# Kernel optimization log

Hardware: AMD Instinct MI355X
Metric: run time of the kernel (lower is better)

## Reference

```python
import jax, jax.numpy as jnp
import numpy as np

N_EMB = 1024
N_HEAD = 16
HD = N_EMB // N_HEAD
ROPE_BASE = 10000.0


def _rope_cos_sin(seq_len, dim, dtype):
    inv_freq = 1.0 / (ROPE_BASE ** (jnp.arange(0, dim, 2, dtype=jnp.float32) / dim))
    t = jnp.arange(seq_len, dtype=jnp.float32)
    freqs = jnp.outer(t, inv_freq)              # [S, dim/2]
    emb = jnp.concatenate([freqs, freqs], -1)    # [S, dim]
    return jnp.cos(emb).astype(dtype), jnp.sin(emb).astype(dtype)


def _rotate_half(x):
    x1, x2 = jnp.split(x, 2, axis=-1)
    return jnp.concatenate([-x2, x1], axis=-1)


def _apply_rope(x):
    # x: [B, H, L, hd]; rotary over sequence axis (-2)
    cos, sin = _rope_cos_sin(x.shape[-2], x.shape[-1], x.dtype)
    return x * cos + _rotate_half(x) * sin


def setup_inputs() -> dict:
    key = jax.random.key(0)
    ks = jax.random.split(key, 8)
    B, T, S = 2, 2048, 2048
    std = 0.02
    return {
        "x": jax.random.normal(ks[0], (B, T, N_EMB), jnp.float32),
        "memory": jax.random.normal(ks[1], (B, S, N_EMB), jnp.float32),
        "q_w": jax.random.normal(ks[2], (N_EMB, N_EMB), jnp.float32) * std,
        "q_b": jnp.zeros((N_EMB,), jnp.float32),
        "kv_w": jax.random.normal(ks[3], (N_EMB, 2 * N_EMB), jnp.float32) * std,
        "kv_b": jnp.zeros((2 * N_EMB,), jnp.float32),
        "proj_w": jax.random.normal(ks[4], (N_EMB, N_EMB), jnp.float32) * std,
        "proj_b": jnp.zeros((N_EMB,), jnp.float32),
    }


def reference(x, memory, q_w, q_b, kv_w, kv_b, proj_w, proj_b):
    B, S, C = memory.shape
    T = x.shape[1]
    kv = memory @ kv_w + kv_b                      # [B,S,2C]
    K, V = jnp.split(kv, 2, axis=-1)
    Q = x @ q_w + q_b                              # [B,T,C]

    def heads(t, L):
        return t.reshape(B, L, N_HEAD, HD).transpose(0, 2, 1, 3)

    Q, K, V = heads(Q, T), heads(K, S), heads(V, S)
    Q = jax.nn.elu(Q) + 1.0                        # positive feature map
    K = jax.nn.elu(K) + 1.0
    Q_rot = _apply_rope(Q)
    K_rot = _apply_rope(K)
    # denom row-sum: sum_s Q.K_s == Q . (sum_s K_s) -- identical math, no SxT matrix
    denom = jnp.einsum('bhtd,bhd->bht', Q, K.sum(axis=2))[..., None]  # [B,H,T,1]
    att = jnp.einsum('bhtd,bhsd->bhts', Q_rot, K_rot) / denom          # [B,H,T,S]
    y = jnp.einsum('bhts,bhsd->bhtd', att, V)                          # [B,H,T,hd]
    y = y.transpose(0, 2, 1, 3).reshape(B, T, C)
    return y @ proj_w + proj_b
```

## Files before the change

kernel.cpp:

```cpp
#include <hip/hip_runtime.h>
#include <cstddef>
#include <cstdint>

#define B_SZ  2
#define T_SEQ 2048
#define S_SEQ 2048
#define C_EMB 1024
#define NH    16
#define HD    64
#define KDIM  1024

typedef __attribute__((ext_vector_type(8))) short bf16x8;
typedef __attribute__((ext_vector_type(4))) float f32x4;

#define OFF_XH    ((size_t)0)
#define OFF_XL    ((size_t)2097152)
#define OFF_MEMH  ((size_t)4194304)
#define OFF_MEML  ((size_t)6291456)
#define OFF_QWH   ((size_t)8388608)
#define OFF_QWL   ((size_t)8912896)
#define OFF_KVWH  ((size_t)9437184)
#define OFF_KVWL  ((size_t)10485760)
#define OFF_PWH   ((size_t)11534336)
#define OFF_PWL   ((size_t)12058624)
#define OFF_KSUM  ((size_t)12582912)
#define OFF_MT    ((size_t)12584960)
#define OFF_TAB   ((size_t)12716032)
#define OFF_YH    ((size_t)12847104)
#define OFF_YL    ((size_t)14944256)
#define WS_FLOATS ((size_t)17041408)

__device__ __forceinline__ float elu1(float v) {
    return v > 0.0f ? v + 1.0f : __expf(v);
}
__device__ __forceinline__ unsigned short bf16_rne(float x) {
    union { float f; unsigned int u; } v; v.f = x;
    unsigned int u = v.u;
    return (unsigned short)((u + 0x7FFFu + ((u >> 16) & 1u)) >> 16);
}
__device__ __forceinline__ float bf16_to_f(unsigned short h) {
    union { unsigned int u; float f; } v; v.u = ((unsigned int)h) << 16;
    return v.f;
}

#define PREP_BLOCKS 13064

__device__ __forceinline__ void split4_body(
    const float4* __restrict__ in, ushort4* __restrict__ hi,
    ushort4* __restrict__ lo, int i)
{
    float4 v = in[i];
    ushort4 h, l;
    h.x = bf16_rne(v.x); l.x = bf16_rne(v.x - bf16_to_f(h.x));
    h.y = bf16_rne(v.y); l.y = bf16_rne(v.y - bf16_to_f(h.y));
    h.z = bf16_rne(v.z); l.z = bf16_rne(v.z - bf16_to_f(h.z));
    h.w = bf16_rne(v.w); l.w = bf16_rne(v.w - bf16_to_f(h.w));
    hi[i] = h; lo[i] = l;
}

__device__ __forceinline__ void transpose_body(
    const float* __restrict__ W, unsigned short* __restrict__ Wth,
    unsigned short* __restrict__ Wtl, int K, int N, int bx, int by,
    float (*tile)[33])
{
    const int k0 = by * 32, n0 = bx * 32;
    const int tx = threadIdx.x & 31, ty = threadIdx.x >> 5;
    #pragma unroll
    for (int j = 0; j < 4; ++j)
        tile[ty + j * 8][tx] = W[(size_t)(k0 + ty + j * 8) * N + n0 + tx];
    __syncthreads();
    #pragma unroll
    for (int j = 0; j < 4; ++j) {
        float x = tile[tx][ty + j * 8];
        unsigned short h = bf16_rne(x);
        unsigned short l = bf16_rne(x - bf16_to_f(h));
        size_t o = (size_t)(n0 + ty + j * 8) * K + k0 + tx;
        Wth[o] = h; Wtl[o] = l;
    }
}

__global__ __launch_bounds__(256) void prep_kernel(
    const float* __restrict__ x, const float* __restrict__ memory,
    const float* __restrict__ q_w, const float* __restrict__ kv_w,
    const float* __restrict__ proj_w,
    unsigned short* __restrict__ xh, unsigned short* __restrict__ xl,
    unsigned short* __restrict__ mh, unsigned short* __restrict__ ml,
    unsigned short* __restrict__ qwh, unsigned short* __restrict__ qwl,
    unsigned short* __restrict__ kvwh, unsigned short* __restrict__ kvwl,
    unsigned short* __restrict__ pwh, unsigned short* __restrict__ pwl,
    float2* __restrict__ tab, float* __restrict__ zero_base)
{
    __shared__ float tile[32][33];
    const int bid = blockIdx.x;
    const int tid = threadIdx.x;
    if (bid < 4096) {
        split4_body((const float4*)x, (ushort4*)xh, (ushort4*)xl, bid * 256 + tid);
    } else if (bid < 8192) {
        split4_body((const float4*)memory, (ushort4*)mh, (ushort4*)ml, (bid - 4096) * 256 + tid);
    } else if (bid < 9216) {
        int i = bid - 8192;
        transpose_body(q_w, qwh, qwl, 1024, 1024, i & 31, i >> 5, tile);
    } else if (bid < 11264) {
        int i = bid - 9216;
        transpose_body(kv_w, kvwh, kvwl, 1024, 2048, i & 63, i >> 6, tile);
    } else if (bid < 12288) {
        int i = bid - 11264;
        transpose_body(proj_w, pwh, pwl, 1024, 1024, i & 31, i >> 5, tile);
    } else if (bid < 12544) {
        int idx = (bid - 12288) * 256 + tid;
        int pos = idx >> 5, i = idx & 31;
        double invf = exp(-(double)i * (9.210340371976184 / 32.0));
        float arg = (float)((double)pos * invf);
        float sn, cs;
        sincosf(arg, &sn, &cs);
        tab[idx] = make_float2(cs, sn);
    } else {
        int idx = (bid - 12544) * 256 + tid;
        if (idx < 2048 + 131072) zero_base[idx] = 0.0f;
    }
}

#define WAITCNT_VM(N) asm volatile("s_waitcnt vmcnt(" #N ")" ::: "memory")
#define WAIT_LGKM0()  asm volatile("s_waitcnt lgkmcnt(0)" ::: "memory")

template<int BN, int M_IT, bool KV>
__device__ __forceinline__ void gemm_pipe(
    const unsigned short* __restrict__ Ah, const unsigned short* __restrict__ Al,
    const unsigned short* __restrict__ Bth, const unsigned short* __restrict__ Btl,
    unsigned short* lds, int m0, int n0, f32x4 (&acc)[M_IT][4])
{
    constexpr int BUFSZ = 16384 + 2 * BN * 32;
    constexpr int NT = KDIM / 32;
    const int tid = threadIdx.x;
    const int w = tid >> 6, lane = tid & 63;
    const int quad = lane >> 4, lrow = lane & 15;
    const int sr = tid >> 2;
    const int g  = (tid & 3) ^ ((tid >> 3) & 3);
    constexpr int WAVES_N = (BN == 128) ? 2 : 1;
    const int wr = (WAVES_N == 2) ? (w >> 1) : w;
    const int wc = (WAVES_N == 2) ? (w & 1) : 0;
    const int rowbase = wr * (M_IT * 16);
    const int colbase = wc * 64;
    const int sw = ((quad ^ ((lrow >> 1) & 3)) << 3);

    const unsigned short* gA0 = Ah + (size_t)(m0 + sr) * KDIM + g * 8;
    const unsigned short* gA1 = Ah + (size_t)(m0 + 128 + sr) * KDIM + g * 8;
    const unsigned short* gA2 = Al + (size_t)(m0 + sr) * KDIM + g * 8;
    const unsigned short* gA3 = Al + (size_t)(m0 + 128 + sr) * KDIM + g * 8;
    const unsigned short* gB0;
    const unsigned short* gB1 = nullptr;
    if constexpr (KV) {
        size_t brow = (size_t)(n0 + sr) + (sr >= 64 ? (size_t)960 : 0);
        gB0 = Bth + brow * KDIM + g * 8;
        gB1 = Btl + brow * KDIM + g * 8;
    } else {
        const unsigned short* bsrc = (w < 4) ? Bth : Btl;
        gB0 = bsrc + (size_t)(n0 + (sr & 63)) * KDIM + g * 8;
    }
    const int lA0 = w * 512;
    const int lA1 = 4096 + w * 512;
    const int lA2 = 8192 + w * 512;
    const int lA3 = 12288 + w * 512;
    int lB0, lB1 = 0;
    if constexpr (KV) {
        lB0 = 16384 + w * 512;
        lB1 = 20480 + w * 512;
    } else {
        lB0 = 16384 + ((w >= 4) ? 2048 : 0) + (w & 3) * 512;
    }

    auto STAGE = [&](unsigned short* buf, int k0) {
        __builtin_amdgcn_global_load_lds(
            (const __attribute__((address_space(1))) unsigned int*)(gA0 + k0),
            (__attribute__((address_space(3))) unsigned int*)(buf + lA0), 16, 0, 0);
        __builtin_amdgcn_global_load_lds(
            (const __attribute__((address_space(1))) unsigned int*)(gA1 + k0),
            (__attribute__((address_space(3))) unsigned int*)(buf + lA1), 16, 0, 0);
        __builtin_amdgcn_global_load_lds(
            (const __attribute__((address_space(1))) unsigned int*)(gA2 + k0),
            (__attribute__((address_space(3))) unsigned int*)(buf + lA2), 16, 0, 0);
        __builtin_amdgcn_global_load_lds(
            (const __attribute__((address_space(1))) unsigned int*)(gA3 + k0),
            (__attribute__((address_space(3))) unsigned int*)(buf + lA3), 16, 0, 0);
        __builtin_amdgcn_global_load_lds(
            (const __attribute__((address_space(1))) unsigned int*)(gB0 + k0),
            (__attribute__((address_space(3))) unsigned int*)(buf + lB0), 16, 0, 0);
        if constexpr (KV)
            __builtin_amdgcn_global_load_lds(
                (const __attribute__((address_space(1))) unsigned int*)(gB1 + k0),
                (__attribute__((address_space(3))) unsigned int*)(buf + lB1), 16, 0, 0);
    };

    unsigned short* cur = lds;
    unsigned short* nxt = lds + BUFSZ;
    unsigned short* thr = lds + 2 * BUFSZ;
    STAGE(cur, 0);
    STAGE(nxt, 32);

    #pragma unroll 1
    for (int t = 0; t < NT; ++t) {
        if (t == NT - 1) {
            WAITCNT_VM(0);
        } else {
            if constexpr (KV) { WAITCNT_VM(6); } else { WAITCNT_VM(5); }
        }
        __builtin_amdgcn_s_barrier();

        bf16x8 ah[M_IT], al[M_IT];
        #pragma unroll
        for (int it = 0; it < M_IT; ++it) {
            int off = (rowbase + it * 16 + lrow) * 32 + sw;
            ah[it] = *(const bf16x8*)&cur[off];
            al[it] = *(const bf16x8*)&cur[8192 + off];
        }
        bf16x8 bh[2], bl[2];
        #pragma unroll
        for (int jt = 0; jt < 2; ++jt) {
            int boff = (colbase + jt * 16 + lrow) * 32 + sw;
            bh[jt] = *(const bf16x8*)&cur[16384 + boff];
            bl[jt] = *(const bf16x8*)&cur[16384 + BN * 32 + boff];
        }
        if (t + 2 < NT) STAGE(thr, (t + 2) * 32);
        __builtin_amdgcn_s_barrier();
        WAIT_LGKM0();
        __builtin_amdgcn_sched_barrier(0);
        __builtin_amdgcn_s_setprio(1);
        #pragma unroll
        for (int it = 0; it < M_IT; ++it)
            #pragma unroll
            for (int jt = 0; jt < 2; ++jt) {
                acc[it][jt] = __builtin_amdgcn_mfma_f32_16x16x32_bf16(ah[it], bh[jt], acc[it][jt], 0, 0, 0);
                acc[it][jt] = __builtin_amdgcn_mfma_f32_16x16x32_bf16(ah[it], bl[jt], acc[it][jt], 0, 0, 0);
                acc[it][jt] = __builtin_amdgcn_mfma_f32_16x16x32_bf16(al[it], bh[jt], acc[it][jt], 0, 0, 0);
            }
        __builtin_amdgcn_s_setprio(0);
        __builtin_amdgcn_s_barrier();

        #pragma unroll
        for (int jt = 0; jt < 2; ++jt) {
            int boff = (colbase + (jt + 2) * 16 + lrow) * 32 + sw;
            bh[jt] = *(const bf16x8*)&cur[16384 + boff];
            bl[jt] = *(const bf16x8*)&cur[16384 + BN * 32 + boff];
        }
        __builtin_amdgcn_s_barrier();
        WAIT_LGKM0();
        __builtin_amdgcn_sched_barrier(0);
        __builtin_amdgcn_s_setprio(1);
        #pragma unroll
        for (int it = 0; it < M_IT; ++it)
            #pragma unroll
            for (int jt = 0; jt < 2; ++jt) {
                acc[it][jt + 2] = __builtin_amdgcn_mfma_f32_16x16x32_bf16(ah[it], bh[jt], acc[it][jt + 2], 0, 0, 0);
                acc[it][jt + 2] = __builtin_amdgcn_mfma_f32_16x16x32_bf16(ah[it], bl[jt], acc[it][jt + 2], 0, 0, 0);
                acc[it][jt + 2] = __builtin_amdgcn_mfma_f32_16x16x32_bf16(al[it], bh[jt], acc[it][jt + 2], 0, 0, 0);
            }
        __builtin_amdgcn_s_setprio(0);

        unsigned short* tmp = cur; cur = nxt; nxt = thr; thr = tmp;
    }
    __syncthreads();
}

__global__ __launch_bounds__(512) void gemm_kv(
    const unsigned short* __restrict__ Ah, const unsigned short* __restrict__ Al,
    const unsigned short* __restrict__ Bth, const unsigned short* __restrict__ Btl,
    const float* __restrict__ bias, const float2* __restrict__ tab,
    float* __restrict__ Ksum, float* __restrict__ Mt)
{
    __shared__ alignas(16) unsigned short smem[73728];
    const int tid = threadIdx.x;
    const int w = tid >> 6, lane = tid & 63;
    const int wr = w >> 1, wc = w & 1;
    const int quad = lane >> 4, lrow = lane & 15;
    const int h  = blockIdx.x;
    const int m0 = blockIdx.y * 256;
    const int b  = m0 >> 11;
    const int tbase = (m0 & 2047) + wr * 64;
    const int bh_idx = b * NH + h;

    f32x4 acc[4][4] = {};
    gemm_pipe<128, 4, true>(Ah, Al, Bth, Btl, smem, m0, h * 64, acc);

    const bool isK = (wc == 0);
    const int colg = (isK ? 0 : C_EMB) + h * 64;
    float bb[4];
    #pragma unroll
    for (int jt = 0; jt < 4; ++jt) bb[jt] = bias[colg + jt * 16 + lrow];
    #pragma unroll
    for (int it = 0; it < 4; ++it)
        #pragma unroll
        for (int jt = 0; jt < 4; ++jt)
            #pragma unroll
            for (int r = 0; r < 4; ++r) {
                float v = acc[it][jt][r] + bb[jt];
                acc[it][jt][r] = isK ? elu1(v) : v;
            }

    if (isK) {
        #pragma unroll
        for (int jt = 0; jt < 4; ++jt) {
            float p = 0.0f;
            #pragma unroll
            for (int it = 0; it < 4; ++it)
                #pragma unroll
                for (int r = 0; r < 4; ++r) p += acc[it][jt][r];
            p += __shfl_xor(p, 16);
            p += __shfl_xor(p, 32);
            if (quad == 0)
                atomicAdd(&Ksum[b * C_EMB + h * 64 + jt * 16 + lrow], p);
        }
        #pragma unroll
        for (int it = 0; it < 4; ++it)
            #pragma unroll
            for (int r = 0; r < 4; ++r) {
                int s = tbase + it * 16 + quad * 4 + r;
                float2 c0 = tab[s * 32 + lrow];
                float2 c1 = tab[s * 32 + 16 + lrow];
                float a0 = acc[it][0][r], a1 = acc[it][1][r];
                float a2 = acc[it][2][r], a3 = acc[it][3][r];
                acc[it][0][r] = a0 * c0.x - a2 * c0.y;
                acc[it][2][r] = a2 * c0.x + a0 * c0.y;
                acc[it][1][r] = a1 * c1.x - a3 * c1.y;
                acc[it][3][r] = a3 * c1.x + a1 * c1.y;
            }
    }

    unsigned short* Hd = smem + (isK ? 0 : 33792);
    unsigned short* Ld = Hd + 16896;
    #pragma unroll
    for (int jt = 0; jt < 4; ++jt) {
        int d = jt * 16 + lrow;
        #pragma unroll
        for (int it = 0; it < 4; ++it) {
            int t0loc = wr * 64 + it * 16 + quad * 4;
            ushort4 h4, l4;
            float v0 = acc[it][jt][0], v1 = acc[it][jt][1];
            float v2 = acc[it][jt][2], v3 = acc[it][jt][3];
            h4.x = bf16_rne(v0); l4.x = bf16_rne(v0 - bf16_to_f(h4.x));
            h4.y = bf16_rne(v1); l4.y = bf16_rne(v1 - bf16_to_f(h4.y));
            h4.z = bf16_rne(v2); l4.z = bf16_rne(v2 - bf16_to_f(h4.z));
            h4.w = bf16_rne(v3); l4.w = bf16_rne(v3 - bf16_to_f(h4.w));
            *(ushort4*)&Hd[d * 264 + t0loc] = h4;
            *(ushort4*)&Ld[d * 264 + t0loc] = l4;
        }
    }
    __syncthreads();

    {
        const unsigned short* KH = smem;
        const unsigned short* KL = smem + 16896;
        const unsigned short* VH = smem + 33792;
        const unsigned short* VL = smem + 50688;
        const int mrow = (w & 3) * 16 + lrow;
        const int thalf = w >> 2;
        f32x4 macc[4] = {};
        #pragma unroll
        for (int ks = 0; ks < 4; ++ks) {
            int kof = thalf * 128 + ks * 32 + quad * 8;
            bf16x8 vah = *(const bf16x8*)&VH[mrow * 264 + kof];
            bf16x8 val = *(const bf16x8*)&VL[mrow * 264 + kof];
            #pragma unroll
            for (int jt = 0; jt < 4; ++jt) {
                int nrow = jt * 16 + lrow;
                bf16x8 kbh = *(const bf16x8*)&KH[nrow * 264 + kof];
                bf16x8 kbl = *(const bf16x8*)&KL[nrow * 264 + kof];
                macc[jt] = __builtin_amdgcn_mfma_f32_16x16x32_bf16(vah, kbh, macc[jt], 0, 0, 0);
                macc[jt] = __builtin_amdgcn_mfma_f32_16x16x32_bf16(vah, kbl, macc[jt], 0, 0, 0);
                macc[jt] = __builtin_amdgcn_mfma_f32_16x16x32_bf16(val, kbh, macc[jt], 0, 0, 0);
            }
        }
        #pragma unroll
        for (int jt = 0; jt < 4; ++jt)
            #pragma unroll
            for (int r = 0; r < 4; ++r)
                atomicAdd(&Mt[((size_t)bh_idx * 64 + (w & 3) * 16 + quad * 4 + r) * 64 + jt * 16 + lrow],
                          macc[jt][r]);
    }
}

__global__ __launch_bounds__(512) void gemm_q(
    const unsigned short* __restrict__ Ah, const unsigned short* __restrict__ Al,
    const unsigned short* __restrict__ Bth, const unsigned short* __restrict__ Btl,
    const float* __restrict__ bias, const float2* __restrict__ tab,
    const float* __restrict__ Ksum, const float* __restrict__ Mt,
    unsigned short* __restrict__ Yh, unsigned short* __restrict__ Yl)
{
    __shared__ alignas(16) unsigned short smem[61440];
    const int h  = blockIdx.x;
    const int m0 = blockIdx.y * 256;
    f32x4 acc[2][4] = {};
    gemm_pipe<64, 2, false>(Ah, Al, Bth, Btl, smem, m0, h * 64, acc);

    const int tid = threadIdx.x;
    const int w = tid >> 6, lane = tid & 63;
    const int quad = lane >> 4, lrow = lane & 15;
    const int b = m0 >> 11;
    const int tbase = (m0 & 2047) + w * 32;
    const int bh = b * NH + h;

    float bb[4];
    #pragma unroll
    for (int jt = 0; jt < 4; ++jt) bb[jt] = bias[h * 64 + jt * 16 + lrow];
    #pragma unroll
    for (int it = 0; it < 2; ++it)
        #pragma unroll
        for (int jt = 0; jt < 4; ++jt)
            #pragma unroll
            for (int r = 0; r < 4; ++r)
                acc[it][jt][r] = elu1(acc[it][jt][r] + bb[jt]);

    float ks[4], den_reg[2][4];
    #pragma unroll
    for (int jt = 0; jt < 4; ++jt) ks[jt] = Ksum[b * C_EMB + h * 64 + jt * 16 + lrow];
    #pragma unroll
    for (int it = 0; it < 2; ++it)
        #pragma unroll
        for (int r = 0; r < 4; ++r) {
            float p = acc[it][0][r] * ks[0] + acc[it][1][r] * ks[1]
                    + acc[it][2][r] * ks[2] + acc[it][3][r] * ks[3];
            p += __shfl_xor(p, 1);
            p += __shfl_xor(p, 2);
            p += __shfl_xor(p, 4);
            p += __shfl_xor(p, 8);
            den_reg[it][r] = p;
        }

    #pragma unroll
    for (int it = 0; it < 2; ++it)
        #pragma unroll
        for (int r = 0; r < 4; ++r) {
            int s = tbase + it * 16 + quad * 4 + r;
            float2 c0 = tab[s * 32 + lrow];
            float2 c1 = tab[s * 32 + 16 + lrow];
            float a0 = acc[it][0][r], a1 = acc[it][1][r];
            float a2 = acc[it][2][r], a3 = acc[it][3][r];
            acc[it][0][r] = a0 * c0.x - a2 * c0.y;
            acc[it][2][r] = a2 * c0.x + a0 * c0.y;
            acc[it][1][r] = a1 * c1.x - a3 * c1.y;
            acc[it][3][r] = a3 * c1.x + a1 * c1.y;
        }

    unsigned short* QH = smem + w * 4608;
    unsigned short* QL = QH + 2304;
    #pragma unroll
    for (int it = 0; it < 2; ++it)
        #pragma unroll
        for (int jt = 0; jt < 4; ++jt)
            #pragma unroll
            for (int r = 0; r < 4; ++r) {
                int tloc = it * 16 + quad * 4 + r;
                int d = jt * 16 + lrow;
                float v = acc[it][jt][r];
                unsigned short hh = bf16_rne(v);
                QH[tloc * 72 + d] = hh;
                QL[tloc * 72 + d] = bf16_rne(v - bf16_to_f(hh));
            }

    f32x4 acc2[2][4] = {};
    #pragma unroll
    for (int kc = 0; kc < 2; ++kc) {
        bf16x8 mbh[4], mbl[4];
        #pragma unroll
        for (int jt2 = 0; jt2 < 4; ++jt2) {
            const float* mp = &Mt[((size_t)bh * 64 + jt2 * 16 + lrow) * 64 + kc * 32 + quad * 8];
            #pragma unroll
            for (int e = 0; e < 8; ++e) {
                float x = mp[e];
                unsigned short hh = bf16_rne(x);
                mbh[jt2][e] = (short)hh;
                mbl[jt2][e] = (short)bf16_rne(x - bf16_to_f(hh));
            }
        }
        #pragma unroll
        for (int it2 = 0; it2 < 2; ++it2) {
            int ro = (it2 * 16 + lrow) * 72 + kc * 32 + quad * 8;
            bf16x8 qh = *(const bf16x8*)&QH[ro];
            bf16x8 ql = *(const bf16x8*)&QL[ro];
            #pragma unroll
            for (int jt2 = 0; jt2 < 4; ++jt2) {
                acc2[it2][jt2] = __builtin_amdgcn_mfma_f32_16x16x32_bf16(qh, mbh[jt2], acc2[it2][jt2], 0, 0, 0);
                acc2[it2][jt2] = __builtin_amdgcn_mfma_f32_16x16x32_bf16(qh, mbl[jt2], acc2[it2][jt2], 0, 0, 0);
                acc2[it2][jt2] = __builtin_amdgcn_mfma_f32_16x16x32_bf16(ql, mbh[jt2], acc2[it2][jt2], 0, 0, 0);
            }
        }
    }

    #pragma unroll
    for (int it2 = 0; it2 < 2; ++it2)
        #pragma unroll
        for (int jt2 = 0; jt2 < 4; ++jt2)
            #pragma unroll
            for (int r = 0; r < 4; ++r) {
                float v = acc2[it2][jt2][r] / den_reg[it2][r];
                size_t o = ((size_t)(m0 + w * 32 + it2 * 16 + quad * 4 + r)) * C_EMB
                         + h * 64 + jt2 * 16 + lrow;
                unsigned short hh = bf16_rne(v);
                Yh[o] = hh;
                Yl[o] = bf16_rne(v - bf16_to_f(hh));
            }
}

__global__ __launch_bounds__(512) void gemm_out(
    const unsigned short* __restrict__ Ah, const unsigned short* __restrict__ Al,
    const unsigned short* __restrict__ Bth, const unsigned short* __restrict__ Btl,
    const float* __restrict__ bias, float* __restrict__ out)
{
    __shared__ alignas(16) unsigned short smem[61440];
    const int m0 = blockIdx.y * 256, n0 = blockIdx.x * 64;
    f32x4 acc[2][4] = {};
    gemm_pipe<64, 2, false>(Ah, Al, Bth, Btl, smem, m0, n0, acc);

    const int tid = threadIdx.x;
    const int w = tid >> 6, lane = tid & 63;
    const int quad = lane >> 4, lrow = lane & 15;

    #pragma unroll
    for (int jt = 0; jt < 4; ++jt) {
        int gc = n0 + jt * 16 + lrow;
        float bb = bias[gc];
        #pragma unroll
        for (int it = 0; it < 2; ++it) {
            int grb = m0 + w * 32 + it * 16 + quad * 4;
            #pragma unroll
            for (int r = 0; r < 4; ++r)
                out[(size_t)(grb + r) * C_EMB + gc] = acc[it][jt][r] + bb;
        }
    }
}

extern "C" void kernel_launch(void* const* d_in, const int* in_sizes, int n_in,
                              void* d_out, int out_size, void* d_ws, size_t ws_size,
                              hipStream_t stream)
{
    const float* x      = (const float*)d_in[0];
    const float* memory = (const float*)d_in[1];
    const float* q_w    = (const float*)d_in[2];
    const float* q_b    = (const float*)d_in[3];
    const float* kv_w   = (const float*)d_in[4];
    const float* kv_b   = (const float*)d_in[5];
    const float* proj_w = (const float*)d_in[6];
    const float* proj_b = (const float*)d_in[7];

    if (ws_size < WS_FLOATS * sizeof(float)) return;

    float* ws = (float*)d_ws;
    unsigned short* xh   = (unsigned short*)(ws + OFF_XH);
    unsigned short* xl   = (unsigned short*)(ws + OFF_XL);
    unsigned short* mh   = (unsigned short*)(ws + OFF_MEMH);
    unsigned short* ml   = (unsigned short*)(ws + OFF_MEML);
    unsigned short* qwh  = (unsigned short*)(ws + OFF_QWH);
    unsigned short* qwl  = (unsigned short*)(ws + OFF_QWL);
    unsigned short* kvwh = (unsigned short*)(ws + OFF_KVWH);
    unsigned short* kvwl = (unsigned short*)(ws + OFF_KVWL);
    unsigned short* pwh  = (unsigned short*)(ws + OFF_PWH);
    unsigned short* pwl  = (unsigned short*)(ws + OFF_PWL);
    unsigned short* Yh   = (unsigned short*)(ws + OFF_YH);
    unsigned short* Yl   = (unsigned short*)(ws + OFF_YL);
    float*  Ksum = ws + OFF_KSUM;
    float*  Mm   = ws + OFF_MT;
    float2* tab  = (float2*)(ws + OFF_TAB);

    prep_kernel<<<PREP_BLOCKS, 256, 0, stream>>>(
        x, memory, q_w, kv_w, proj_w,
        xh, xl, mh, ml, qwh, qwl, kvwh, kvwl, pwh, pwl,
        tab, Ksum );

    gemm_kv<<<dim3(16, 16), 512, 0, stream>>>(mh, ml, kvwh, kvwl, kv_b, tab, Ksum, Mm);
    gemm_q<<<dim3(16, 16), 512, 0, stream>>>(xh, xl, qwh, qwl, q_b, tab, Ksum, Mm, Yh, Yl);
    gemm_out<<<dim3(16, 16), 512, 0, stream>>>(Yh, Yl, pwh, pwl, proj_b, (float*)d_out);
}
```

Before: 234.5 us.

## Load all B fragments up front, drop inner barriers, swizzle blocks across XCDs

The GEMM main loop now issues all four B-fragment LDS reads at once and uses partial lgkmcnt waits, so the first half of the MFMAs overlaps with the remaining reads. This removes two intra-iteration block barriers and reorders the MFMAs so they are grouped by operand pair. Separately, block indices are remapped so that tiles sharing the same A or B rows land on the same XCD, which should improve L2 reuse. The cost is more live registers for the B fragments, and the swizzle assumes a 16-wide by 16-tall grid.

```diff
diff --git a/kernel.cpp b/kernel.cpp
--- a/kernel.cpp
+++ b/kernel.cpp
@@ -120,8 +120,9 @@
     }
 }
 
-#define WAITCNT_VM(N) asm volatile("s_waitcnt vmcnt(" #N ")" ::: "memory")
-#define WAIT_LGKM0()  asm volatile("s_waitcnt lgkmcnt(0)" ::: "memory")
+#define WAITCNT_VM(N)   asm volatile("s_waitcnt vmcnt(" #N ")" ::: "memory")
+#define WAITCNT_LGKM(N) asm volatile("s_waitcnt lgkmcnt(" #N ")" ::: "memory")
+#define CBAR()          asm volatile("" ::: "memory")
 
 template<int BN, int M_IT, bool KV>
 __device__ __forceinline__ void gemm_pipe(
@@ -206,59 +207,76 @@
         }
         __builtin_amdgcn_s_barrier();
 
-        bf16x8 ah[M_IT], al[M_IT];
+        bf16x8 ah[M_IT], al[M_IT], bh[4], bl[4];
         #pragma unroll
         for (int it = 0; it < M_IT; ++it) {
             int off = (rowbase + it * 16 + lrow) * 32 + sw;
             ah[it] = *(const bf16x8*)&cur[off];
             al[it] = *(const bf16x8*)&cur[8192 + off];
         }
-        bf16x8 bh[2], bl[2];
         #pragma unroll
         for (int jt = 0; jt < 2; ++jt) {
             int boff = (colbase + jt * 16 + lrow) * 32 + sw;
             bh[jt] = *(const bf16x8*)&cur[16384 + boff];
             bl[jt] = *(const bf16x8*)&cur[16384 + BN * 32 + boff];
         }
+        CBAR();
+        #pragma unroll
+        for (int jt = 2; jt < 4; ++jt) {
+            int boff = (colbase + jt * 16 + lrow) * 32 + sw;
+            bh[jt] = *(const bf16x8*)&cur[16384 + boff];
+            bl[jt] = *(const bf16x8*)&cur[16384 + BN * 32 + boff];
+        }
         if (t + 2 < NT) STAGE(thr, (t + 2) * 32);
-        __builtin_amdgcn_s_barrier();
-        WAIT_LGKM0();
+
+        WAITCNT_LGKM(4);
         __builtin_amdgcn_sched_barrier(0);
         __builtin_amdgcn_s_setprio(1);
         #pragma unroll
         for (int it = 0; it < M_IT; ++it)
             #pragma unroll
-            for (int jt = 0; jt < 2; ++jt) {
+            for (int jt = 0; jt < 2; ++jt)
                 acc[it][jt] = __builtin_amdgcn_mfma_f32_16x16x32_bf16(ah[it], bh[jt], acc[it][jt], 0, 0, 0);
+        #pragma unroll
+        for (int it = 0; it < M_IT; ++it)
+            #pragma unroll
+            for (int jt = 0; jt < 2; ++jt)
                 acc[it][jt] = __builtin_amdgcn_mfma_f32_16x16x32_bf16(ah[it], bl[jt], acc[it][jt], 0, 0, 0);
+        #pragma unroll
+        for (int it = 0; it < M_IT; ++it)
+            #pragma unroll
+            for (int jt = 0; jt < 2; ++jt)
                 acc[it][jt] = __builtin_amdgcn_mfma_f32_16x16x32_bf16(al[it], bh[jt], acc[it][jt], 0, 0, 0);
-            }
+
+        WAITCNT_LGKM(0);
+        __builtin_amdgcn_sched_barrier(0);
+        #pragma unroll
+        for (int it = 0; it < M_IT; ++it)
+            #pragma unroll
+            for (int jt = 2; jt < 4; ++jt)
+                acc[it][jt] = __builtin_amdgcn_mfma_f32_16x16x32_bf16(ah[it], bh[jt], acc[it][jt], 0, 0, 0);
+        #pragma unroll
+        for (int it = 0; it < M_IT; ++it)
+            #pragma unroll
+            for (int jt = 2; jt < 4; ++jt)
+                acc[it][jt] = __builtin_amdgcn_mfma_f32_16x16x32_bf16(ah[it], bl[jt], acc[it][jt], 0, 0, 0);
+        #pragma unroll
+        for (int it = 0; it < M_IT; ++it)
+            #pragma unroll
+            for (int jt = 2; jt < 4; ++jt)
+                acc[it][jt] = __builtin_amdgcn_mfma_f32_16x16x32_bf16(al[it], bh[jt], acc[it][jt], 0, 0, 0);
         __builtin_amdgcn_s_setprio(0);
-        __builtin_amdgcn_s_barrier();
-
-        #pragma unroll
-        for (int jt = 0; jt < 2; ++jt) {
-            int boff = (colbase + (jt + 2) * 16 + lrow) * 32 + sw;
-            bh[jt] = *(const bf16x8*)&cur[16384 + boff];
-            bl[jt] = *(const bf16x8*)&cur[16384 + BN * 32 + boff];
-        }
-        __builtin_amdgcn_s_barrier();
-        WAIT_LGKM0();
-        __builtin_amdgcn_sched_barrier(0);
-        __builtin_amdgcn_s_setprio(1);
-        #pragma unroll
-        for (int it = 0; it < M_IT; ++it)
-            #pragma unroll
-            for (int jt = 0; jt < 2; ++jt) {
-                acc[it][jt + 2] = __builtin_amdgcn_mfma_f32_16x16x32_bf16(ah[it], bh[jt], acc[it][jt + 2], 0, 0, 0);
-                acc[it][jt + 2] = __builtin_amdgcn_mfma_f32_16x16x32_bf16(ah[it], bl[jt], acc[it][jt + 2], 0, 0, 0);
-                acc[it][jt + 2] = __builtin_amdgcn_mfma_f32_16x16x32_bf16(al[it], bh[jt], acc[it][jt + 2], 0, 0, 0);
-            }
-        __builtin_amdgcn_s_setprio(0);
 
         unsigned short* tmp = cur; cur = nxt; nxt = thr; thr = tmp;
     }
     __syncthreads();
+}
+
+__device__ __forceinline__ void xcd_swz16(int& bx, int& by) {
+    int id = (int)(blockIdx.x + (blockIdx.y << 4));
+    int x = id & 7, k = id >> 3;
+    bx = k >> 1;
+    by = x * 2 + (k & 1);
 }
 
 __global__ __launch_bounds__(512) void gemm_kv(
@@ -272,8 +290,9 @@
     const int w = tid >> 6, lane = tid & 63;
     const int wr = w >> 1, wc = w & 1;
     const int quad = lane >> 4, lrow = lane & 15;
-    const int h  = blockIdx.x;
-    const int m0 = blockIdx.y * 256;
+    int h, mt;
+    xcd_swz16(h, mt);
+    const int m0 = mt * 256;
     const int b  = m0 >> 11;
     const int tbase = (m0 & 2047) + wr * 64;
     const int bh_idx = b * NH + h;
@@ -386,8 +405,9 @@
     unsigned short* __restrict__ Yh, unsigned short* __restrict__ Yl)
 {
     __shared__ alignas(16) unsigned short smem[61440];
-    const int h  = blockIdx.x;
-    const int m0 = blockIdx.y * 256;
+    int h, mt;
+    xcd_swz16(h, mt);
+    const int m0 = mt * 256;
     f32x4 acc[2][4] = {};
     gemm_pipe<64, 2, false>(Ah, Al, Bth, Btl, smem, m0, h * 64, acc);
 
@@ -506,7 +526,9 @@
     const float* __restrict__ bias, float* __restrict__ out)
 {
     __shared__ alignas(16) unsigned short smem[61440];
-    const int m0 = blockIdx.y * 256, n0 = blockIdx.x * 64;
+    int nt, mt;
+    xcd_swz16(nt, mt);
+    const int m0 = mt * 256, n0 = nt * 64;
     f32x4 acc[2][4] = {};
     gemm_pipe<64, 2, false>(Ah, Al, Bth, Btl, smem, m0, n0, acc);
 
```

After: 222.4 us. -5.2%, faster.
